# Performance work log

Measured on AMD Instinct MI355X. Metric: run time of the kernel, lower is better.

Reference implementation:

```python
import jax, jax.numpy as jnp
import numpy as np

N_NODES = 20000
N_EDGES = 320000
IN_CH = 64
OUT_CH = 64
HEADS = 4
NEG_SLOPE = 0.2
BN_EPS = 1e-5


def setup_inputs() -> dict:
    key = jax.random.key(0)
    ks = jax.random.split(key, 12)
    x = jax.random.normal(ks[0], (N_NODES, IN_CH), dtype=jnp.float32)
    embedding = jax.random.normal(ks[1], (N_NODES, OUT_CH), dtype=jnp.float32)
    # random edges guaranteed to have no self loops (module removes them anyway)
    src = jax.random.randint(ks[2], (N_EDGES,), 0, N_NODES, dtype=jnp.int32)
    off = jax.random.randint(ks[3], (N_EDGES,), 1, N_NODES, dtype=jnp.int32)
    dst = (src + off) % N_NODES
    edge_index = jnp.stack([src, dst], axis=0)  # [2, E]
    glorot = lambda k, shape: jax.random.uniform(k, shape, jnp.float32, -1.0, 1.0) * np.sqrt(6.0 / (shape[-2] * shape[-1] if len(shape) > 1 else shape[-1]))
    W = glorot(ks[4], (IN_CH, HEADS * OUT_CH))            # lin weight (no bias)
    att_i = glorot(ks[5], (1, HEADS, OUT_CH))
    att_j = glorot(ks[6], (1, HEADS, OUT_CH))
    att_em_i = glorot(ks[7], (1, HEADS, OUT_CH)) * 0.1    # zeros at init; random for test coverage
    att_em_j = glorot(ks[8], (1, HEADS, OUT_CH)) * 0.1
    bias = jnp.zeros((OUT_CH,), jnp.float32)
    gamma = jnp.ones((OUT_CH,), jnp.float32)
    beta = jnp.zeros((OUT_CH,), jnp.float32)
    return {"x": x, "edge_index": edge_index, "embedding": embedding, "W": W,
            "att_i": att_i, "att_j": att_j, "att_em_i": att_em_i, "att_em_j": att_em_j,
            "bias": bias, "gamma": gamma, "beta": beta}


def _gnn_forward(x, edge_index, embedding, W, att_i, att_j, att_em_i, att_em_j,
                 bias, gamma, beta):
    N = x.shape[0]
    H, C = att_i.shape[1], att_i.shape[2]
    # add self loops (input edges contain none by construction)
    loops = jnp.arange(N, dtype=edge_index.dtype)
    src = jnp.concatenate([edge_index[0], loops])  # x_j / embedding_j index
    dst = jnp.concatenate([edge_index[1], loops])  # x_i / embedding_i index (edge_index_i)
    xl = (x @ W).reshape(N, H, C)                  # [N,H,C]
    # attention logits decompose per node: <x, att> + <emb, att_em>
    logit_i = jnp.einsum('nhc,hc->nh', xl, att_i[0]) + jnp.einsum('nc,hc->nh', embedding, att_em_i[0])
    logit_j = jnp.einsum('nhc,hc->nh', xl, att_j[0]) + jnp.einsum('nc,hc->nh', embedding, att_em_j[0])
    alpha = logit_i[dst] + logit_j[src]            # [Etot,H]
    alpha = jnp.where(alpha >= 0, alpha, NEG_SLOPE * alpha)  # leaky_relu
    # segment softmax over destination node (PyG softmax)
    amax = jax.ops.segment_max(alpha, dst, num_segments=N)   # every node has a self loop
    alpha = jnp.exp(alpha - amax[dst])
    denom = jax.ops.segment_sum(alpha, dst, num_segments=N)
    alpha = alpha / (denom[dst] + 1e-16)
    # weighted message aggregation (scatter-add)
    msg = alpha[:, :, None] * xl[src]              # [Etot,H,C]
    out = jax.ops.segment_sum(msg, dst, num_segments=N)      # [N,H,C]
    out = out.mean(axis=1) + bias                  # concat=False -> head mean
    # BatchNorm1d (training-mode batch statistics) + ReLU
    mu = out.mean(axis=0)
    var = jnp.mean((out - mu) ** 2, axis=0)
    out = (out - mu) * jax.lax.rsqrt(var + BN_EPS) * gamma + beta
    return jax.nn.relu(out)


def reference(x, edge_index, embedding, W, att_i, att_j, att_em_i, att_em_j, bias, gamma, beta):
    return _gnn_forward(x, edge_index, embedding, W, att_i, att_j, att_em_i, att_em_j, bias, gamma, beta)
```

## Files before the change

kernel.cpp:

```cpp
#include <hip/hip_runtime.h>
#include <hip/hip_fp16.h>
#include <math.h>

#define N_NODES 20000
#define N_EDGES 320000
#define N_TOT (N_EDGES + N_NODES)
#define IN_CH 64
#define OUT_CH 64
#define HEADS 4
#define HC (HEADS * OUT_CH)
#define NEG_SLOPE 0.2f
#define BN_EPS 1e-5f
#define BN_SLOTS 64
#define CAP 64

__global__ __launch_bounds__(256) void k_xl(
    const float* __restrict__ x, const float* __restrict__ W,
    const float* __restrict__ emb, const float* __restrict__ att_i,
    const float* __restrict__ att_j, const float* __restrict__ att_em_i,
    const float* __restrict__ att_em_j, __half* __restrict__ xlh,
    float* __restrict__ logit_i, float* __restrict__ logit_j,
    int* __restrict__ cnt, float* __restrict__ bnp) {
    __shared__ float xs[16][64];
    const int t = threadIdx.x;
    const int lane = t & 63, w = t >> 6;
    const int node0 = blockIdx.x * 16;
    const int gtid = blockIdx.x * 256 + t;

    if (gtid < N_NODES) cnt[gtid] = 0;
    if (gtid < BN_SLOTS * 128) bnp[gtid] = 0.f;

    {
        int n = t >> 4, c4 = (t & 15) * 4;
        float4 v = *(const float4*)&x[(node0 + n) * IN_CH + c4];
        *(float4*)&xs[n][c4] = v;
    }
    float wcol[64];
#pragma unroll
    for (int k = 0; k < 64; ++k) wcol[k] = W[k * HC + t];
    const float ai = att_i[t], aj = att_j[t];
    const float aei = att_em_i[t], aej = att_em_j[t];
    __syncthreads();

    for (int n = 0; n < 16; ++n) {
        const int gn = node0 + n;
        float acc = 0.f;
        const float4* xr = (const float4*)xs[n];
#pragma unroll
        for (int k4 = 0; k4 < 16; ++k4) {
            float4 xv = xr[k4];
            acc += xv.x * wcol[4 * k4] + xv.y * wcol[4 * k4 + 1] +
                   xv.z * wcol[4 * k4 + 2] + xv.w * wcol[4 * k4 + 3];
        }
        xlh[gn * HC + t] = __float2half(acc);
        float e = emb[gn * OUT_CH + lane];
        float li = acc * ai + e * aei;
        float lj = acc * aj + e * aej;
#pragma unroll
        for (int o = 32; o > 0; o >>= 1) {
            li += __shfl_xor(li, o, 64);
            lj += __shfl_xor(lj, o, 64);
        }
        if (lane == 0) {
            logit_i[gn * HEADS + w] = li;
            logit_j[gn * HEADS + w] = lj;
        }
    }
}

__global__ __launch_bounds__(256) void k_bucket(
    const int* __restrict__ srcA, const int* __restrict__ dstA,
    const float* __restrict__ logit_i, const float* __restrict__ logit_j,
    int* __restrict__ cnt, int* __restrict__ bS, float4* __restrict__ bW) {
    const int e = blockIdx.x * 256 + threadIdx.x;
    if (e >= N_TOT) return;
    int s, d;
    if (e < N_EDGES) {
        s = srcA[e];
        d = dstA[e];
    } else {
        s = d = e - N_EDGES;
    }
    int pos = atomicAdd(&cnt[d], 1);
    if (pos >= CAP) return;
    const float4 li = *(const float4*)&logit_i[d * HEADS];
    const float4 lj = *(const float4*)&logit_j[s * HEADS];
    float4 wv;
    float a;
    a = li.x + lj.x; a = (a >= 0.f) ? a : NEG_SLOPE * a; wv.x = __expf(a);
    a = li.y + lj.y; a = (a >= 0.f) ? a : NEG_SLOPE * a; wv.y = __expf(a);
    a = li.z + lj.z; a = (a >= 0.f) ? a : NEG_SLOPE * a; wv.z = __expf(a);
    a = li.w + lj.w; a = (a >= 0.f) ? a : NEG_SLOPE * a; wv.w = __expf(a);
    const int slot = d * CAP + pos;
    bS[slot] = s;
    bW[slot] = wv;
}

__global__ __launch_bounds__(256) void k_node(
    const __half* __restrict__ xlh, const int* __restrict__ cnt,
    const int* __restrict__ bS, const float* __restrict__ bWf,
    const float* __restrict__ bias, float* __restrict__ tmp,
    float* __restrict__ bnp) {
    const int t = threadIdx.x;
    const int wv = t >> 6, lane = t & 63;
    const int n = blockIdx.x * 4 + wv;
    const int m = min(cnt[n], CAP);
    const int h = lane >> 4;
    const int nb = n * CAP;

    float4 acc = {0.f, 0.f, 0.f, 0.f};
    float ssum = 0.f;

#pragma unroll 8
    for (int i = 0; i < m; ++i) {
        int s = bS[nb + i];
        float wgt = bWf[(nb + i) * 4 + h];
        ushort4 r = *(const ushort4*)(xlh + (size_t)s * HC + lane * 4);
        ssum += wgt;
        acc.x += wgt * __half2float(__ushort_as_half(r.x));
        acc.y += wgt * __half2float(__ushort_as_half(r.y));
        acc.z += wgt * __half2float(__ushort_as_half(r.z));
        acc.w += wgt * __half2float(__ushort_as_half(r.w));
    }
    const float inv = 1.f / ssum;
    acc.x *= inv; acc.y *= inv; acc.z *= inv; acc.w *= inv;
#pragma unroll
    for (int o = 16; o <= 32; o <<= 1) {
        acc.x += __shfl_xor(acc.x, o, 64);
        acc.y += __shfl_xor(acc.y, o, 64);
        acc.z += __shfl_xor(acc.z, o, 64);
        acc.w += __shfl_xor(acc.w, o, 64);
    }
    __shared__ float rows[4][64];
    if (lane < 16) {
        int c = lane * 4;
        float4 b = *(const float4*)&bias[c];
        float4 o4 = {0.25f * acc.x + b.x, 0.25f * acc.y + b.y,
                     0.25f * acc.z + b.z, 0.25f * acc.w + b.w};
        *(float4*)&tmp[n * OUT_CH + c] = o4;
        *(float4*)&rows[wv][c] = o4;
    }
    __syncthreads();
    if (t < 64) {
        float s = 0.f, ss = 0.f;
#pragma unroll
        for (int r = 0; r < 4; ++r) {
            float v = rows[r][t];
            s += v;
            ss += v * v;
        }
        int slot = (blockIdx.x & (BN_SLOTS - 1)) * 128;
        atomicAdd(&bnp[slot + t], s);
        atomicAdd(&bnp[slot + 64 + t], ss);
    }
}

__global__ __launch_bounds__(256) void k_final(const float* __restrict__ tmp,
                                               const float* __restrict__ bnp,
                                               const float* __restrict__ gamma,
                                               const float* __restrict__ beta,
                                               float* __restrict__ out) {
    __shared__ float sscale[64], sshift[64];
    const int t = threadIdx.x;
    if (t < 64) {
        float s = 0.f, ss = 0.f;
#pragma unroll
        for (int k = 0; k < BN_SLOTS; ++k) {
            s += bnp[k * 128 + t];
            ss += bnp[k * 128 + 64 + t];
        }
        const float invN = 1.f / (float)N_NODES;
        float mu = s * invN;
        float var = ss * invN - mu * mu;
        float sc = rsqrtf(var + BN_EPS) * gamma[t];
        sscale[t] = sc;
        sshift[t] = beta[t] - mu * sc;
    }
    __syncthreads();
    const float4* t4 = (const float4*)tmp;
    float4* o4 = (float4*)out;
    const int total4 = N_NODES * OUT_CH / 4;
    for (int i = blockIdx.x * 256 + t; i < total4; i += gridDim.x * 256) {
        int c = (i & 15) * 4;
        float4 v = t4[i];
        float4 r;
        r.x = fmaxf(v.x * sscale[c] + sshift[c], 0.f);
        r.y = fmaxf(v.y * sscale[c + 1] + sshift[c + 1], 0.f);
        r.z = fmaxf(v.z * sscale[c + 2] + sshift[c + 2], 0.f);
        r.w = fmaxf(v.w * sscale[c + 3] + sshift[c + 3], 0.f);
        o4[i] = r;
    }
}

extern "C" void kernel_launch(void* const* d_in, const int* in_sizes, int n_in,
                              void* d_out, int out_size, void* d_ws,
                              size_t ws_size, hipStream_t stream) {
    const float* x = (const float*)d_in[0];
    const int* ei = (const int*)d_in[1];
    const float* emb = (const float*)d_in[2];
    const float* W = (const float*)d_in[3];
    const float* att_i = (const float*)d_in[4];
    const float* att_j = (const float*)d_in[5];
    const float* att_em_i = (const float*)d_in[6];
    const float* att_em_j = (const float*)d_in[7];
    const float* bias = (const float*)d_in[8];
    const float* gamma = (const float*)d_in[9];
    const float* beta = (const float*)d_in[10];
    float* out = (float*)d_out;

    const int* srcA = ei;
    const int* dstA = ei + N_EDGES;

    char* p = (char*)d_ws;
    auto alloc = [&](size_t bytes) {
        char* r = p;
        p += (bytes + 255) & ~size_t(255);
        return r;
    };
    __half* xlh = (__half*)alloc(sizeof(__half) * N_NODES * HC);
    float* lgi = (float*)alloc(sizeof(float) * N_NODES * HEADS);
    float* lgj = (float*)alloc(sizeof(float) * N_NODES * HEADS);
    float* tmp = (float*)alloc(sizeof(float) * N_NODES * OUT_CH);
    float* bnp = (float*)alloc(sizeof(float) * BN_SLOTS * 128);
    int* cnt = (int*)alloc(sizeof(int) * N_NODES);
    int* bS = (int*)alloc(sizeof(int) * N_NODES * CAP);
    float4* bW = (float4*)alloc(sizeof(float4) * N_NODES * CAP);
    (void)alloc(4096);

    k_xl<<<N_NODES / 16, 256, 0, stream>>>(x, W, emb, att_i, att_j, att_em_i,
                                           att_em_j, xlh, lgi, lgj, cnt, bnp);
    k_bucket<<<(N_TOT + 255) / 256, 256, 0, stream>>>(srcA, dstA, lgi, lgj,
                                                      cnt, bS, bW);
    k_node<<<N_NODES / 4, 256, 0, stream>>>(xlh, cnt, bS, (const float*)bW,
                                            bias, tmp, bnp);
    k_final<<<256, 256, 0, stream>>>(tmp, bnp, gamma, beta, out);
}
```

Before: 169.4 us.

## Fuse all stages into one persistent kernel with grid-wide barriers

Replaces the four separate kernel launches with a single persistent 512-block kernel that runs projection, edge bucketing, node aggregation and batch-norm finalisation as phases separated by atomic spin-wait grid barriers. Aggregated rows stay in shared memory until the final BN/ReLU pass, so the intermediate tmp buffer round trip through global memory goes away. The aim is to remove launch gaps and that extra traffic. In exchange the grid is much smaller, which lowers parallelism in the gather phase. Correctness relies on every block being co-resident, and the barrier uses a bounded spin with a magic-value handshake that could misbehave across calls.

```diff
diff --git a/kernel.cpp b/kernel.cpp
--- a/kernel.cpp
+++ b/kernel.cpp
@@ -13,155 +13,198 @@
 #define BN_EPS 1e-5f
 #define BN_SLOTS 64
 #define CAP 64
-
-__global__ __launch_bounds__(256) void k_xl(
+#define NBLK 512
+#define MAGIC 0x5EEDBEEF
+#define SPIN_CAP (1 << 22)
+
+__device__ __forceinline__ void gbar(int* bar, int target) {
+    __syncthreads();
+    if (threadIdx.x == 0) {
+        int spins = 0;
+        while (__hip_atomic_load(&bar[0], __ATOMIC_ACQUIRE,
+                                 __HIP_MEMORY_SCOPE_AGENT) != MAGIC &&
+               spins < SPIN_CAP) {
+            ++spins;
+            __builtin_amdgcn_s_sleep(1);
+        }
+        __threadfence();
+        __hip_atomic_fetch_add(&bar[1], 1, __ATOMIC_ACQ_REL,
+                               __HIP_MEMORY_SCOPE_AGENT);
+        spins = 0;
+        while (__hip_atomic_load(&bar[1], __ATOMIC_ACQUIRE,
+                                 __HIP_MEMORY_SCOPE_AGENT) < target &&
+               spins < SPIN_CAP) {
+            ++spins;
+            __builtin_amdgcn_s_sleep(1);
+        }
+        __threadfence();
+    }
+    __syncthreads();
+}
+
+__global__ __launch_bounds__(256, 2) void k_mega(
     const float* __restrict__ x, const float* __restrict__ W,
     const float* __restrict__ emb, const float* __restrict__ att_i,
     const float* __restrict__ att_j, const float* __restrict__ att_em_i,
-    const float* __restrict__ att_em_j, __half* __restrict__ xlh,
-    float* __restrict__ logit_i, float* __restrict__ logit_j,
-    int* __restrict__ cnt, float* __restrict__ bnp) {
+    const float* __restrict__ att_em_j, const int* __restrict__ srcA,
+    const int* __restrict__ dstA, const float* __restrict__ bias,
+    const float* __restrict__ gamma, const float* __restrict__ beta,
+    __half* __restrict__ xlh, float* __restrict__ lgi,
+    float* __restrict__ lgj, int* __restrict__ cnt, int* __restrict__ bS,
+    float4* __restrict__ bW, float* __restrict__ bnp, int* __restrict__ bar,
+    float* __restrict__ out) {
+    const int t = threadIdx.x;
+    const int lane = t & 63, wv = t >> 6;
+    const int bid = blockIdx.x;
+
     __shared__ float xs[16][64];
-    const int t = threadIdx.x;
-    const int lane = t & 63, w = t >> 6;
-    const int node0 = blockIdx.x * 16;
-    const int gtid = blockIdx.x * 256 + t;
-
-    if (gtid < N_NODES) cnt[gtid] = 0;
-    if (gtid < BN_SLOTS * 128) bnp[gtid] = 0.f;
-
-    {
-        int n = t >> 4, c4 = (t & 15) * 4;
-        float4 v = *(const float4*)&x[(node0 + n) * IN_CH + c4];
-        *(float4*)&xs[n][c4] = v;
-    }
+    __shared__ float obuf[40][64];
+    __shared__ float rows[4][64];
+    __shared__ float sscale[64], sshift[64];
+
+    if (bid == 0 && t == 0) {
+        __hip_atomic_store(&bar[1], 0, __ATOMIC_RELAXED,
+                           __HIP_MEMORY_SCOPE_AGENT);
+        __hip_atomic_store(&bar[0], MAGIC, __ATOMIC_RELEASE,
+                           __HIP_MEMORY_SCOPE_AGENT);
+    }
+
+    for (int i = bid * 256 + t; i < N_NODES; i += NBLK * 256) cnt[i] = 0;
+    for (int i = bid * 256 + t; i < BN_SLOTS * 128; i += NBLK * 256)
+        bnp[i] = 0.f;
+
     float wcol[64];
 #pragma unroll
     for (int k = 0; k < 64; ++k) wcol[k] = W[k * HC + t];
     const float ai = att_i[t], aj = att_j[t];
     const float aei = att_em_i[t], aej = att_em_j[t];
-    __syncthreads();
-
-    for (int n = 0; n < 16; ++n) {
-        const int gn = node0 + n;
-        float acc = 0.f;
-        const float4* xr = (const float4*)xs[n];
-#pragma unroll
-        for (int k4 = 0; k4 < 16; ++k4) {
-            float4 xv = xr[k4];
-            acc += xv.x * wcol[4 * k4] + xv.y * wcol[4 * k4 + 1] +
-                   xv.z * wcol[4 * k4 + 2] + xv.w * wcol[4 * k4 + 3];
-        }
-        xlh[gn * HC + t] = __float2half(acc);
-        float e = emb[gn * OUT_CH + lane];
-        float li = acc * ai + e * aei;
-        float lj = acc * aj + e * aej;
-#pragma unroll
-        for (int o = 32; o > 0; o >>= 1) {
-            li += __shfl_xor(li, o, 64);
-            lj += __shfl_xor(lj, o, 64);
-        }
-        if (lane == 0) {
-            logit_i[gn * HEADS + w] = li;
-            logit_j[gn * HEADS + w] = lj;
-        }
-    }
-}
-
-__global__ __launch_bounds__(256) void k_bucket(
-    const int* __restrict__ srcA, const int* __restrict__ dstA,
-    const float* __restrict__ logit_i, const float* __restrict__ logit_j,
-    int* __restrict__ cnt, int* __restrict__ bS, float4* __restrict__ bW) {
-    const int e = blockIdx.x * 256 + threadIdx.x;
-    if (e >= N_TOT) return;
-    int s, d;
-    if (e < N_EDGES) {
-        s = srcA[e];
-        d = dstA[e];
-    } else {
-        s = d = e - N_EDGES;
-    }
-    int pos = atomicAdd(&cnt[d], 1);
-    if (pos >= CAP) return;
-    const float4 li = *(const float4*)&logit_i[d * HEADS];
-    const float4 lj = *(const float4*)&logit_j[s * HEADS];
-    float4 wv;
-    float a;
-    a = li.x + lj.x; a = (a >= 0.f) ? a : NEG_SLOPE * a; wv.x = __expf(a);
-    a = li.y + lj.y; a = (a >= 0.f) ? a : NEG_SLOPE * a; wv.y = __expf(a);
-    a = li.z + lj.z; a = (a >= 0.f) ? a : NEG_SLOPE * a; wv.z = __expf(a);
-    a = li.w + lj.w; a = (a >= 0.f) ? a : NEG_SLOPE * a; wv.w = __expf(a);
-    const int slot = d * CAP + pos;
-    bS[slot] = s;
-    bW[slot] = wv;
-}
-
-__global__ __launch_bounds__(256) void k_node(
-    const __half* __restrict__ xlh, const int* __restrict__ cnt,
-    const int* __restrict__ bS, const float* __restrict__ bWf,
-    const float* __restrict__ bias, float* __restrict__ tmp,
-    float* __restrict__ bnp) {
-    const int t = threadIdx.x;
-    const int wv = t >> 6, lane = t & 63;
-    const int n = blockIdx.x * 4 + wv;
-    const int m = min(cnt[n], CAP);
+
+    for (int tile = bid; tile < N_NODES / 16; tile += NBLK) {
+        const int node0 = tile * 16;
+        __syncthreads();
+        {
+            int n = t >> 4, c4 = (t & 15) * 4;
+            float4 v = *(const float4*)&x[(node0 + n) * IN_CH + c4];
+            *(float4*)&xs[n][c4] = v;
+        }
+        __syncthreads();
+        for (int n = 0; n < 16; ++n) {
+            const int gn = node0 + n;
+            float acc = 0.f;
+            const float4* xr = (const float4*)xs[n];
+#pragma unroll
+            for (int k4 = 0; k4 < 16; ++k4) {
+                float4 xv = xr[k4];
+                acc += xv.x * wcol[4 * k4] + xv.y * wcol[4 * k4 + 1] +
+                       xv.z * wcol[4 * k4 + 2] + xv.w * wcol[4 * k4 + 3];
+            }
+            xlh[gn * HC + t] = __float2half(acc);
+            float e = emb[gn * OUT_CH + lane];
+            float li = acc * ai + e * aei;
+            float lj = acc * aj + e * aej;
+#pragma unroll
+            for (int o = 32; o > 0; o >>= 1) {
+                li += __shfl_xor(li, o, 64);
+                lj += __shfl_xor(lj, o, 64);
+            }
+            if (lane == 0) {
+                lgi[gn * HEADS + wv] = li;
+                lgj[gn * HEADS + wv] = lj;
+            }
+        }
+    }
+    gbar(bar, NBLK);
+
+    for (int e = bid * 256 + t; e < N_TOT; e += NBLK * 256) {
+        int s, d;
+        if (e < N_EDGES) {
+            s = srcA[e];
+            d = dstA[e];
+        } else {
+            s = d = e - N_EDGES;
+        }
+        int pos = atomicAdd(&cnt[d], 1);
+        if (pos < CAP) {
+            const float4 li4 = *(const float4*)&lgi[d * HEADS];
+            const float4 lj4 = *(const float4*)&lgj[s * HEADS];
+            float4 w4;
+            float a;
+            a = li4.x + lj4.x; a = (a >= 0.f) ? a : NEG_SLOPE * a; w4.x = __expf(a);
+            a = li4.y + lj4.y; a = (a >= 0.f) ? a : NEG_SLOPE * a; w4.y = __expf(a);
+            a = li4.z + lj4.z; a = (a >= 0.f) ? a : NEG_SLOPE * a; w4.z = __expf(a);
+            a = li4.w + lj4.w; a = (a >= 0.f) ? a : NEG_SLOPE * a; w4.w = __expf(a);
+            const int slot = d * CAP + pos;
+            bS[slot] = s;
+            bW[slot] = w4;
+        }
+    }
+    gbar(bar, 2 * NBLK);
+
+    const float* bWf = (const float*)bW;
     const int h = lane >> 4;
-    const int nb = n * CAP;
-
-    float4 acc = {0.f, 0.f, 0.f, 0.f};
-    float ssum = 0.f;
-
+    float accS = 0.f, accSS = 0.f;
+    for (int it = 0; it < 10; ++it) {
+        const int n = it * (NBLK * 4) + bid * 4 + wv;
+        const bool valid = (n < N_NODES);
+        if (valid) {
+            const int m = min(cnt[n], CAP);
+            const int nb = n * CAP;
+            float4 acc = {0.f, 0.f, 0.f, 0.f};
+            float ssum = 0.f;
 #pragma unroll 8
-    for (int i = 0; i < m; ++i) {
-        int s = bS[nb + i];
-        float wgt = bWf[(nb + i) * 4 + h];
-        ushort4 r = *(const ushort4*)(xlh + (size_t)s * HC + lane * 4);
-        ssum += wgt;
-        acc.x += wgt * __half2float(__ushort_as_half(r.x));
-        acc.y += wgt * __half2float(__ushort_as_half(r.y));
-        acc.z += wgt * __half2float(__ushort_as_half(r.z));
-        acc.w += wgt * __half2float(__ushort_as_half(r.w));
-    }
-    const float inv = 1.f / ssum;
-    acc.x *= inv; acc.y *= inv; acc.z *= inv; acc.w *= inv;
-#pragma unroll
-    for (int o = 16; o <= 32; o <<= 1) {
-        acc.x += __shfl_xor(acc.x, o, 64);
-        acc.y += __shfl_xor(acc.y, o, 64);
-        acc.z += __shfl_xor(acc.z, o, 64);
-        acc.w += __shfl_xor(acc.w, o, 64);
-    }
-    __shared__ float rows[4][64];
-    if (lane < 16) {
-        int c = lane * 4;
-        float4 b = *(const float4*)&bias[c];
-        float4 o4 = {0.25f * acc.x + b.x, 0.25f * acc.y + b.y,
-                     0.25f * acc.z + b.z, 0.25f * acc.w + b.w};
-        *(float4*)&tmp[n * OUT_CH + c] = o4;
-        *(float4*)&rows[wv][c] = o4;
-    }
-    __syncthreads();
+            for (int i = 0; i < m; ++i) {
+                int s = bS[nb + i];
+                float wgt = bWf[(nb + i) * 4 + h];
+                ushort4 r = *(const ushort4*)(xlh + (size_t)s * HC + lane * 4);
+                ssum += wgt;
+                acc.x += wgt * __half2float(__ushort_as_half(r.x));
+                acc.y += wgt * __half2float(__ushort_as_half(r.y));
+                acc.z += wgt * __half2float(__ushort_as_half(r.z));
+                acc.w += wgt * __half2float(__ushort_as_half(r.w));
+            }
+            const float inv = 1.f / ssum;
+            acc.x *= inv; acc.y *= inv; acc.z *= inv; acc.w *= inv;
+#pragma unroll
+            for (int o = 16; o <= 32; o <<= 1) {
+                acc.x += __shfl_xor(acc.x, o, 64);
+                acc.y += __shfl_xor(acc.y, o, 64);
+                acc.z += __shfl_xor(acc.z, o, 64);
+                acc.w += __shfl_xor(acc.w, o, 64);
+            }
+            if (lane < 16) {
+                int c = lane * 4;
+                float4 b = *(const float4*)&bias[c];
+                float4 o4 = {0.25f * acc.x + b.x, 0.25f * acc.y + b.y,
+                             0.25f * acc.z + b.z, 0.25f * acc.w + b.w};
+                *(float4*)&rows[wv][c] = o4;
+                *(float4*)&obuf[it * 4 + wv][c] = o4;
+            }
+        } else if (lane < 16) {
+            int c = lane * 4;
+            float4 z = {0.f, 0.f, 0.f, 0.f};
+            *(float4*)&rows[wv][c] = z;
+        }
+        __syncthreads();
+        if (t < 64) {
+            float s = 0.f, ss = 0.f;
+#pragma unroll
+            for (int r = 0; r < 4; ++r) {
+                float v = rows[r][t];
+                s += v;
+                ss += v * v;
+            }
+            accS += s;
+            accSS += ss;
+        }
+        __syncthreads();
+    }
     if (t < 64) {
-        float s = 0.f, ss = 0.f;
-#pragma unroll
-        for (int r = 0; r < 4; ++r) {
-            float v = rows[r][t];
-            s += v;
-            ss += v * v;
-        }
-        int slot = (blockIdx.x & (BN_SLOTS - 1)) * 128;
-        atomicAdd(&bnp[slot + t], s);
-        atomicAdd(&bnp[slot + 64 + t], ss);
-    }
-}
-
-__global__ __launch_bounds__(256) void k_final(const float* __restrict__ tmp,
-                                               const float* __restrict__ bnp,
-                                               const float* __restrict__ gamma,
-                                               const float* __restrict__ beta,
-                                               float* __restrict__ out) {
-    __shared__ float sscale[64], sshift[64];
-    const int t = threadIdx.x;
+        int slot = (bid & (BN_SLOTS - 1)) * 128;
+        atomicAdd(&bnp[slot + t], accS);
+        atomicAdd(&bnp[slot + 64 + t], accSS);
+    }
+    gbar(bar, 3 * NBLK);
+
     if (t < 64) {
         float s = 0.f, ss = 0.f;
 #pragma unroll
@@ -177,18 +220,13 @@
         sshift[t] = beta[t] - mu * sc;
     }
     __syncthreads();
-    const float4* t4 = (const float4*)tmp;
-    float4* o4 = (float4*)out;
-    const int total4 = N_NODES * OUT_CH / 4;
-    for (int i = blockIdx.x * 256 + t; i < total4; i += gridDim.x * 256) {
-        int c = (i & 15) * 4;
-        float4 v = t4[i];
-        float4 r;
-        r.x = fmaxf(v.x * sscale[c] + sshift[c], 0.f);
-        r.y = fmaxf(v.y * sscale[c + 1] + sshift[c + 1], 0.f);
-        r.z = fmaxf(v.z * sscale[c + 2] + sshift[c + 2], 0.f);
-        r.w = fmaxf(v.w * sscale[c + 3] + sshift[c + 3], 0.f);
-        o4[i] = r;
+    for (int it = 0; it < 10; ++it) {
+        const int n = it * (NBLK * 4) + bid * 4 + wv;
+        if (n < N_NODES) {
+            float v = obuf[it * 4 + wv][lane];
+            v = v * sscale[lane] + sshift[lane];
+            out[n * OUT_CH + lane] = fmaxf(v, 0.f);
+        }
     }
 }
 
@@ -220,18 +258,14 @@
     __half* xlh = (__half*)alloc(sizeof(__half) * N_NODES * HC);
     float* lgi = (float*)alloc(sizeof(float) * N_NODES * HEADS);
     float* lgj = (float*)alloc(sizeof(float) * N_NODES * HEADS);
-    float* tmp = (float*)alloc(sizeof(float) * N_NODES * OUT_CH);
     float* bnp = (float*)alloc(sizeof(float) * BN_SLOTS * 128);
     int* cnt = (int*)alloc(sizeof(int) * N_NODES);
     int* bS = (int*)alloc(sizeof(int) * N_NODES * CAP);
     float4* bW = (float4*)alloc(sizeof(float4) * N_NODES * CAP);
+    int* bar = (int*)alloc(256);
     (void)alloc(4096);
 
-    k_xl<<<N_NODES / 16, 256, 0, stream>>>(x, W, emb, att_i, att_j, att_em_i,
-                                           att_em_j, xlh, lgi, lgj, cnt, bnp);
-    k_bucket<<<(N_TOT + 255) / 256, 256, 0, stream>>>(srcA, dstA, lgi, lgj,
-                                                      cnt, bS, bW);
-    k_node<<<N_NODES / 4, 256, 0, stream>>>(xlh, cnt, bS, (const float*)bW,
-                                            bias, tmp, bnp);
-    k_final<<<256, 256, 0, stream>>>(tmp, bnp, gamma, beta, out);
+    k_mega<<<NBLK, 256, 0, stream>>>(x, W, emb, att_i, att_j, att_em_i,
+                                     att_em_j, srcA, dstA, bias, gamma, beta,
+                                     xlh, lgi, lgj, cnt, bS, bW, bnp, bar, out);
 }
```

New measurement: 466.0 us. +175.0%, slower.
